# Performance work log

Hardware: AMD Instinct MI355X
Metric: run time of the kernel (lower is better)

The kernel has to match this reference:

```python
import jax, jax.numpy as jnp
import numpy as np

V, D, H, DH, F, L, B, S = 1400, 1024, 16, 64, 4096, 12, 1, 2048
EPS = 1e-5
STD = 0.02


def _layernorm(x, scale, bias):
    m = jnp.mean(x, axis=-1, keepdims=True)
    v = jnp.var(x, axis=-1, keepdims=True)
    return (x - m) * jax.lax.rsqrt(v + EPS) * scale + bias


def _rope_cache(seq_len, d_head):
    inv_freq = 1.0 / (10000.0 ** (jnp.arange(0, d_head, 2, dtype=jnp.float32) / d_head))
    t = jnp.arange(seq_len, dtype=jnp.float32)
    freqs = jnp.outer(t, inv_freq)              # [S, DH/2]
    emb = jnp.concatenate([freqs, freqs], -1)   # [S, DH]
    return jnp.cos(emb), jnp.sin(emb)


def _rotate_half(x):
    x1, x2 = x[..., : x.shape[-1] // 2], x[..., x.shape[-1] // 2 :]
    return jnp.concatenate([-x2, x1], axis=-1)


def _block(x, p, cos, sin, mask):
    Wq, Wk, Wv, Wo, l1s, l1b, l2s, l2b, w1, w2, w3 = p
    b, s, _ = x.shape
    h = _layernorm(x, l1s, l1b)
    q = jnp.einsum('bsd,de->bse', h, Wq).reshape(b, s, H, DH).transpose(0, 2, 1, 3)
    k = jnp.einsum('bsd,de->bse', h, Wk).reshape(b, s, H, DH).transpose(0, 2, 1, 3)
    v = jnp.einsum('bsd,de->bse', h, Wv).reshape(b, s, H, DH).transpose(0, 2, 1, 3)
    c = cos[None, None]  # [1,1,S,DH]
    sn = sin[None, None]
    q = q * c + _rotate_half(q) * sn
    k = k * c + _rotate_half(k) * sn
    scores = jnp.einsum('bhqd,bhkd->bhqk', q, k) / np.sqrt(DH).astype(np.float32)
    scores = jnp.where(mask, scores, -1e9)
    attn = jax.nn.softmax(scores, axis=-1)      # dropout=identity (eval)
    out = jnp.einsum('bhqk,bhkd->bhqd', attn, v)
    out = out.transpose(0, 2, 1, 3).reshape(b, s, D)
    x = x + jnp.einsum('bsd,de->bse', out, Wo)
    h2 = _layernorm(x, l2s, l2b)
    ffn = jnp.einsum('bsf,fd->bsd', jax.nn.silu(jnp.einsum('bsd,df->bsf', h2, w1)) * jnp.einsum('bsd,df->bsf', h2, w3), w2)
    return x + ffn


def _forward(input_ids, tok_emb, Wq, Wk, Wv, Wo, ln1_s, ln1_b, ln2_s, ln2_b, w1, w2, w3, lnf_s, lnf_b, lm_head):
    b, s = input_ids.shape
    x = tok_emb[input_ids]                      # [B,S,D]
    cos, sin = _rope_cache(s, DH)
    mask = jnp.tril(jnp.ones((s, s), dtype=bool))
    blk = jax.checkpoint(lambda c, p: _block(c, p, cos, sin, mask))
    x, _ = jax.lax.scan(lambda c, p: (blk(c, p), None), x,
                        (Wq, Wk, Wv, Wo, ln1_s, ln1_b, ln2_s, ln2_b, w1, w2, w3))
    x = _layernorm(x, lnf_s, lnf_b)
    return jnp.einsum('bsd,dv->bsv', x, lm_head)


def setup_inputs() -> dict:
    key = jax.random.key(0)
    ks = jax.random.split(key, 10)
    inp = {
        'input_ids': jax.random.randint(ks[0], (B, S), 0, V),
        'tok_emb': jax.random.normal(ks[1], (V, D), jnp.float32) * STD,
        'Wq': jax.random.normal(ks[2], (L, D, D), jnp.float32) * STD,
        'Wk': jax.random.normal(ks[3], (L, D, D), jnp.float32) * STD,
        'Wv': jax.random.normal(ks[4], (L, D, D), jnp.float32) * STD,
        'Wo': jax.random.normal(ks[5], (L, D, D), jnp.float32) * STD,
        'ln1_s': jnp.ones((L, D), jnp.float32),
        'ln1_b': jnp.zeros((L, D), jnp.float32),
        'ln2_s': jnp.ones((L, D), jnp.float32),
        'ln2_b': jnp.zeros((L, D), jnp.float32),
        'w1': jax.random.normal(ks[6], (L, D, F), jnp.float32) * STD,
        'w2': jax.random.normal(ks[7], (L, F, D), jnp.float32) * STD,
        'w3': jax.random.normal(ks[8], (L, D, F), jnp.float32) * STD,
        'lnf_s': jnp.ones((D,), jnp.float32),
        'lnf_b': jnp.zeros((D,), jnp.float32),
        'lm_head': jax.random.normal(ks[9], (D, V), jnp.float32) * STD,
    }
    return inp


def reference(input_ids, tok_emb, Wq, Wk, Wv, Wo, ln1_s, ln1_b, ln2_s, ln2_b, w1, w2, w3, lnf_s, lnf_b, lm_head):
    return _forward(input_ids, tok_emb, Wq, Wk, Wv, Wo, ln1_s, ln1_b, ln2_s, ln2_b, w1, w2, w3, lnf_s, lnf_b, lm_head)
```

## Files before the change

### kernel.cpp

```cpp
#include <hip/hip_runtime.h>
#include <math.h>

constexpr int SEQ = 2048;
constexpr int DIM = 1024;
constexpr int NH  = 16;
constexpr int HD  = 64;
constexpr int FF  = 4096;
constexpr int NL  = 12;
constexpr int VOC = 1400;
constexpr int VOCP = 1408;

typedef __bf16 bf16_t;
typedef __bf16 bf16x8 __attribute__((ext_vector_type(8)));
typedef float  f32x4  __attribute__((ext_vector_type(4)));

typedef __attribute__((address_space(1))) const void GV;
typedef __attribute__((address_space(3))) void LV;

__device__ __forceinline__ void gll16(const bf16_t* g, bf16_t* l) {
  __builtin_amdgcn_global_load_lds((GV*)g, (LV*)l, 16, 0, 0);
}

__global__ __launch_bounds__(256) void k_embed(const int* __restrict__ ids,
                                               const float* __restrict__ emb,
                                               float* __restrict__ x) {
  int s = blockIdx.x;
  int d = threadIdx.x * 4;
  const float4 v = *(const float4*)&emb[(size_t)ids[s] * DIM + d];
  *(float4*)&x[(size_t)s * DIM + d] = v;
}

__global__ __launch_bounds__(256) void k_rtab(float* __restrict__ ct,
                                              float* __restrict__ st) {
  int id = blockIdx.x * 256 + threadIdx.x;
  int i = id & 31;
  int s = id >> 5;
  float ang = (float)s * powf(10000.f, -(float)i * (1.f / 32.f));
  float sn, cs;
  sincosf(ang, &sn, &cs);
  ct[id] = cs;
  st[id] = sn;
}

__global__ __launch_bounds__(256) void k_ln(const float* __restrict__ x,
                                            const float* __restrict__ sc,
                                            const float* __restrict__ bi,
                                            bf16_t* __restrict__ out) {
  int s = blockIdx.x * 4 + (threadIdx.x >> 6);
  int l = threadIdx.x & 63;
  const float* xr = x + (size_t)s * DIM;
  float4 v[4];
  float sum = 0.f, sq = 0.f;
#pragma unroll
  for (int i = 0; i < 4; ++i) {
    v[i] = *(const float4*)&xr[i * 256 + l * 4];
#pragma unroll
    for (int j = 0; j < 4; ++j) { sum += v[i][j]; sq += v[i][j] * v[i][j]; }
  }
#pragma unroll
  for (int d = 1; d < 64; d <<= 1) {
    sum += __shfl_xor(sum, d);
    sq  += __shfl_xor(sq, d);
  }
  float mean = sum * (1.f / DIM);
  float var  = sq * (1.f / DIM) - mean * mean;
  float inv  = rsqrtf(var + 1e-5f);
#pragma unroll
  for (int i = 0; i < 4; ++i) {
    int off = i * 256 + l * 4;
    float4 scv = *(const float4*)&sc[off];
    float4 biv = *(const float4*)&bi[off];
#pragma unroll
    for (int j = 0; j < 4; ++j) {
      float o = (v[i][j] - mean) * inv * scv[j] + biv[j];
      out[(size_t)s * DIM + off + j] = (bf16_t)o;
    }
  }
}

__global__ __launch_bounds__(256) void k_cvt_t(const float* __restrict__ src,
                                               bf16_t* __restrict__ dst,
                                               int K_, int N_, int Npad_,
                                               size_t dstride, int imode) {
  __shared__ bf16_t T[64][66];
  const int k0 = blockIdx.y * 64;
  const int n0 = blockIdx.x * 64;
  const size_t so = (size_t)blockIdx.z * K_ * N_;
  const size_t dof = (size_t)blockIdx.z * dstride;
  const int t = threadIdx.x;
  const int kk = t >> 4;
  const int nn = (t & 15) * 4;
#pragma unroll
  for (int it = 0; it < 4; ++it) {
    int krow = kk + it * 16;
    float4 v = {0.f, 0.f, 0.f, 0.f};
    if (n0 + nn < N_) v = *(const float4*)&src[so + (size_t)(k0 + krow) * N_ + n0 + nn];
#pragma unroll
    for (int q = 0; q < 4; ++q) T[nn + q][krow] = (bf16_t)v[q];
  }
  __syncthreads();
#pragma unroll
  for (int it = 0; it < 4; ++it) {
    int c = it * 256 + t;
    int nr = c >> 4;
    int kc = (c & 15) * 4;
    int f = n0 + nr;
    int drow = (imode == 0) ? f : ((f >> 4) * 32 + ((imode == 2) ? 16 : 0) + (f & 15));
    ushort4 o = *(const ushort4*)&T[nr][kc];
    *(ushort4*)&dst[dof + (size_t)drow * K_ + k0 + kc] = o;
  }
}

template <int TM, int TN, int OUTMODE>
__global__ __launch_bounds__(256) void k_gemm2(const bf16_t* __restrict__ A,
                                               const bf16_t* __restrict__ Bt,
                                               float* __restrict__ Cf,
                                               bf16_t* __restrict__ Cb,
                                               bf16_t* __restrict__ aux1,
                                               bf16_t* __restrict__ aux2,
                                               const float* __restrict__ ct,
                                               const float* __restrict__ st,
                                               int M, int N, int K) {
  constexpr int MI = TM / 32;
  constexpr int JN = TN / 32;
  __shared__ bf16_t As[TM * 64];
  __shared__ bf16_t Bs[TN * 64];
  const int t = threadIdx.x;
  const int w = t >> 6, l = t & 63;
  const int h = l >> 4, r16 = l & 15;
  const int m0 = blockIdx.y * TM, n0 = blockIdx.x * TN;
  const int wr = (w >> 1) * (TM / 2);
  const int wc = (w & 1) * (TN / 2);
  const int sr8  = l >> 3;
  const int xch  = ((l & 7) ^ sr8) * 8;
  const int s7   = r16 & 7;

  f32x4 acc[MI][JN] = {};

  const bf16_t* pa = &A[(size_t)(m0 + w * 8 + sr8) * K + xch];
  const bf16_t* pb = &Bt[(size_t)(n0 + w * 8 + sr8) * K + xch];

  for (int k0 = 0; k0 < K; k0 += 64) {
#pragma unroll
    for (int i = 0; i < MI; ++i)
      gll16(pa + (size_t)i * 32 * K + k0, &As[(i * 32 + w * 8) * 64]);
#pragma unroll
    for (int i = 0; i < JN; ++i)
      gll16(pb + (size_t)i * 32 * K + k0, &Bs[(i * 32 + w * 8) * 64]);
    __syncthreads();
#pragma unroll
    for (int kk = 0; kk < 2; ++kk) {
      const int p = ((kk * 4 + h) ^ s7) * 8;
      bf16x8 af[MI], bfr[JN];
#pragma unroll
      for (int i = 0; i < MI; ++i)
        af[i] = *(const bf16x8*)&As[(wr + i * 16 + r16) * 64 + p];
#pragma unroll
      for (int j = 0; j < JN; ++j)
        bfr[j] = *(const bf16x8*)&Bs[(wc + j * 16 + r16) * 64 + p];
#pragma unroll
      for (int i = 0; i < MI; ++i)
#pragma unroll
        for (int j = 0; j < JN; ++j)
          acc[i][j] = __builtin_amdgcn_mfma_f32_16x16x32_bf16(af[i], bfr[j], acc[i][j], 0, 0, 0);
    }
    __syncthreads();
  }

  if constexpr (OUTMODE == 4) {
    const int reg = n0 >> 10;
    const int cbase = (n0 & 1023) + wc;
    if (reg == 2) {
#pragma unroll
      for (int i = 0; i < MI; ++i)
#pragma unroll
        for (int j = 0; j < JN; ++j)
#pragma unroll
          for (int r = 0; r < 4; ++r) {
            int row = m0 + wr + i * 16 + h * 4 + r;
            Cb[(size_t)row * DIM + cbase + j * 16 + r16] = (bf16_t)acc[i][j][r];
          }
    } else {
      bf16_t* dst = reg ? aux2 : aux1;
#pragma unroll
      for (int i = 0; i < MI; ++i)
#pragma unroll
        for (int r = 0; r < 4; ++r) {
          int row = m0 + wr + i * 16 + h * 4 + r;
          float c0 = ct[row * 32 + r16],      s0 = st[row * 32 + r16];
          float c1 = ct[row * 32 + 16 + r16], s1 = st[row * 32 + 16 + r16];
          float lo0 = acc[i][0][r], hi0 = acc[i][2][r];
          float lo1 = acc[i][1][r], hi1 = acc[i][3][r];
          size_t rb = (size_t)row * DIM + cbase;
          dst[rb + r16]      = (bf16_t)(lo0 * c0 - hi0 * s0);
          dst[rb + 32 + r16] = (bf16_t)(hi0 * c0 + lo0 * s0);
          dst[rb + 16 + r16] = (bf16_t)(lo1 * c1 - hi1 * s1);
          dst[rb + 48 + r16] = (bf16_t)(hi1 * c1 + lo1 * s1);
        }
    }
  } else if constexpr (OUTMODE == 6) {
    const int fbase = ((n0 + wc) >> 5) * 16;
#pragma unroll
    for (int i = 0; i < MI; ++i)
#pragma unroll
      for (int r = 0; r < 4; ++r) {
        int row = m0 + wr + i * 16 + h * 4 + r;
        float a0 = acc[i][0][r], b0 = acc[i][1][r];
        float a1 = acc[i][2][r], b1 = acc[i][3][r];
        float g0 = a0 / (1.f + expf(-a0)) * b0;
        float g1v = a1 / (1.f + expf(-a1)) * b1;
        size_t rb = (size_t)row * FF + fbase;
        aux1[rb + r16]      = (bf16_t)g0;
        aux1[rb + 16 + r16] = (bf16_t)g1v;
      }
  } else {
#pragma unroll
    for (int i = 0; i < MI; ++i)
#pragma unroll
      for (int j = 0; j < JN; ++j)
#pragma unroll
        for (int r = 0; r < 4; ++r) {
          int row = m0 + wr + i * 16 + h * 4 + r;
          int col = n0 + wc + j * 16 + r16;
          if (col < N) {
            float vv = acc[i][j][r];
            size_t idx = (size_t)row * N + col;
            if (OUTMODE == 0) Cf[idx] = vv;
            else Cf[idx] += vv;
          }
        }
  }
}

__global__ __launch_bounds__(512, 1) void k_gemm256_gate(const bf16_t* __restrict__ A,
                                                         const bf16_t* __restrict__ Bt,
                                                         bf16_t* __restrict__ gate,
                                                         int K) {
  __shared__ bf16_t As[2][256 * 64];
  __shared__ bf16_t Bs[2][256 * 64];
  const int t = threadIdx.x;
  const int w = t >> 6, l = t & 63;
  const int h = l >> 4, r16 = l & 15;
  const int m0 = blockIdx.y * 256, n0 = blockIdx.x * 256;
  const int wr = (w >> 2) * 128;
  const int wc = (w & 3) * 64;
  const int sr = t >> 3;
  const int xch = ((t & 7) ^ (sr & 7)) * 8;
  const int s7 = r16 & 7;

  f32x4 acc[8][4] = {};

  const bf16_t* pa = &A[(size_t)(m0 + sr) * K + xch];
  const bf16_t* pb = &Bt[(size_t)(n0 + sr) * K + xch];
  const int NT = K >> 6;

  auto STAGE = [&](int kt, int b) {
    const int k0 = kt << 6;
    bf16_t* baseA = &As[b][(w * 8) * 64];
    bf16_t* baseB = &Bs[b][(w * 8) * 64];
#pragma unroll
    for (int i = 0; i < 4; ++i) {
      gll16(pa + (size_t)(i * 64) * K + k0, baseA + i * 64 * 64);
      gll16(pb + (size_t)(i * 64) * K + k0, baseB + i * 64 * 64);
    }
  };

  STAGE(0, 0);
  asm volatile("s_waitcnt vmcnt(0)" ::: "memory");
  __builtin_amdgcn_s_barrier();
  __builtin_amdgcn_sched_barrier(0);

  int cur = 0;
  for (int tt = 0; tt < NT; ++tt) {
    if (tt + 1 < NT) STAGE(tt + 1, cur ^ 1);
#pragma unroll
    for (int kk = 0; kk < 2; ++kk) {
      const int p = ((kk * 4 + h) ^ s7) * 8;
      bf16x8 af[8], bfr[4];
#pragma unroll
      for (int i = 0; i < 8; ++i)
        af[i] = *(const bf16x8*)&As[cur][(wr + i * 16 + r16) * 64 + p];
#pragma unroll
      for (int j = 0; j < 4; ++j)
        bfr[j] = *(const bf16x8*)&Bs[cur][(wc + j * 16 + r16) * 64 + p];
#pragma unroll
      for (int i = 0; i < 8; ++i)
#pragma unroll
        for (int j = 0; j < 4; ++j)
          acc[i][j] = __builtin_amdgcn_mfma_f32_16x16x32_bf16(af[i], bfr[j], acc[i][j], 0, 0, 0);
    }
    asm volatile("s_waitcnt vmcnt(0)" ::: "memory");
    __builtin_amdgcn_s_barrier();
    __builtin_amdgcn_sched_barrier(0);
    cur ^= 1;
  }

  const int fbase = ((n0 + wc) >> 5) * 16;
#pragma unroll
  for (int i = 0; i < 8; ++i)
#pragma unroll
    for (int r = 0; r < 4; ++r) {
      int row = m0 + wr + i * 16 + h * 4 + r;
      float a0 = acc[i][0][r], b0 = acc[i][1][r];
      float a1 = acc[i][2][r], b1 = acc[i][3][r];
      float g0 = a0 / (1.f + expf(-a0)) * b0;
      float g1v = a1 / (1.f + expf(-a1)) * b1;
      size_t rb = (size_t)row * FF + fbase;
      gate[rb + r16]      = (bf16_t)g0;
      gate[rb + 16 + r16] = (bf16_t)g1v;
    }
}

__global__ __launch_bounds__(256) void k_attn4(const bf16_t* __restrict__ qb,
                                               const bf16_t* __restrict__ kb,
                                               const bf16_t* __restrict__ vb,
                                               bf16_t* __restrict__ ao) {
  __shared__ bf16_t Ks[64][72];
  __shared__ bf16_t Vt[64][72];
  __shared__ bf16_t Pl[4][16][72];
  const int raw = blockIdx.x;
  const int head = blockIdx.y;
  const int qt = (head < 8) ? raw : (31 - raw);
  const int t = threadIdx.x;
  const int w = t >> 6, l = t & 63;
  const int h = l >> 4, r16 = l & 15;
  const size_t hoff = (size_t)head * HD;
  const int srow = t >> 2;
  const int ssg  = (t & 3) * 8;

  const int q0 = qt * 64 + w * 16;
  const int q_abs = q0 + r16;

  bf16x8 aq[2];
#pragma unroll
  for (int c = 0; c < 2; ++c)
    aq[c] = *(const bf16x8*)&qb[(size_t)(q0 + r16) * DIM + hoff + c * 32 + h * 8];

  f32x4 o[4] = {};
  float mrun = -1e30f, lrun = 0.f;

  const int kend = qt * 64 + 63;
  for (int k0 = 0; k0 <= kend; k0 += 64) {
#pragma unroll
    for (int it = 0; it < 2; ++it) {
      bf16x8 kv = *(const bf16x8*)&kb[(size_t)(k0 + srow) * DIM + hoff + ssg + it * 32];
      *(bf16x8*)&Ks[srow][ssg + it * 32] = kv;
    }
#pragma unroll
    for (int it = 0; it < 2; ++it) {
      bf16x8 vv = *(const bf16x8*)&vb[(size_t)(k0 + srow) * DIM + hoff + ssg + it * 32];
#pragma unroll
      for (int j = 0; j < 8; ++j) Vt[ssg + it * 32 + j][srow] = vv[j];
    }
    __syncthreads();

    if (k0 <= q0 + 15) {
      f32x4 sc[4];
      __builtin_amdgcn_s_setprio(1);
#pragma unroll
      for (int tc = 0; tc < 4; ++tc) {
        f32x4 z = {};
        bf16x8 a0 = *(const bf16x8*)&Ks[tc * 16 + r16][h * 8];
        bf16x8 a1 = *(const bf16x8*)&Ks[tc * 16 + r16][32 + h * 8];
        z = __builtin_amdgcn_mfma_f32_16x16x32_bf16(a0, aq[0], z, 0, 0, 0);
        z = __builtin_amdgcn_mfma_f32_16x16x32_bf16(a1, aq[1], z, 0, 0, 0);
        sc[tc] = z;
      }
      __builtin_amdgcn_s_setprio(0);
      float pmax = -1e30f;
#pragma unroll
      for (int tc = 0; tc < 4; ++tc)
#pragma unroll
        for (int r = 0; r < 4; ++r) {
          int key = k0 + tc * 16 + h * 4 + r;
          float v = sc[tc][r] * 0.125f;
          if (key > q_abs) v = -1e30f;
          sc[tc][r] = v;
          pmax = fmaxf(pmax, v);
        }
      pmax = fmaxf(pmax, __shfl_xor(pmax, 16));
      pmax = fmaxf(pmax, __shfl_xor(pmax, 32));
      float mnew = fmaxf(mrun, pmax);
      float alpha = expf(mrun - mnew);
      mrun = mnew;
      float ssum = 0.f;
#pragma unroll
      for (int tc = 0; tc < 4; ++tc)
#pragma unroll
        for (int r = 0; r < 4; ++r) {
          float pv = expf(sc[tc][r] - mnew);
          sc[tc][r] = pv;
          ssum += pv;
        }
      ssum += __shfl_xor(ssum, 16);
      ssum += __shfl_xor(ssum, 32);
      lrun = lrun * alpha + ssum;
#pragma unroll
      for (int tc = 0; tc < 4; ++tc)
#pragma unroll
        for (int r = 0; r < 4; ++r)
          Pl[w][r16][tc * 16 + h * 4 + r] = (bf16_t)sc[tc][r];
      float ar[4];
#pragma unroll
      for (int r = 0; r < 4; ++r) ar[r] = __shfl(alpha, h * 4 + r);
#pragma unroll
      for (int cti = 0; cti < 4; ++cti)
#pragma unroll
        for (int r = 0; r < 4; ++r) o[cti][r] *= ar[r];
      bf16x8 pa0 = *(const bf16x8*)&Pl[w][r16][h * 8];
      bf16x8 pa1 = *(const bf16x8*)&Pl[w][r16][32 + h * 8];
      __builtin_amdgcn_s_setprio(1);
#pragma unroll
      for (int cti = 0; cti < 4; ++cti) {
        bf16x8 v0 = *(const bf16x8*)&Vt[cti * 16 + r16][h * 8];
        bf16x8 v1 = *(const bf16x8*)&Vt[cti * 16 + r16][32 + h * 8];
        o[cti] = __builtin_amdgcn_mfma_f32_16x16x32_bf16(pa0, v0, o[cti], 0, 0, 0);
        o[cti] = __builtin_amdgcn_mfma_f32_16x16x32_bf16(pa1, v1, o[cti], 0, 0, 0);
      }
      __builtin_amdgcn_s_setprio(0);
    }
    __syncthreads();
  }
  float lr[4];
#pragma unroll
  for (int r = 0; r < 4; ++r) lr[r] = __shfl(lrun, h * 4 + r);
#pragma unroll
  for (int cti = 0; cti < 4; ++cti)
#pragma unroll
    for (int r = 0; r < 4; ++r) {
      int row = q0 + h * 4 + r;
      ao[(size_t)row * DIM + hoff + cti * 16 + r16] = (bf16_t)(o[cti][r] / lr[r]);
    }
}

extern "C" void kernel_launch(void* const* d_in, const int* in_sizes, int n_in,
                              void* d_out, int out_size, void* d_ws, size_t ws_size,
                              hipStream_t stream) {
  const int*   ids  = (const int*)d_in[0];
  const float* temb = (const float*)d_in[1];
  const float* Wq   = (const float*)d_in[2];
  const float* Wk   = (const float*)d_in[3];
  const float* Wv   = (const float*)d_in[4];
  const float* Wo   = (const float*)d_in[5];
  const float* ln1s = (const float*)d_in[6];
  const float* ln1b = (const float*)d_in[7];
  const float* ln2s = (const float*)d_in[8];
  const float* ln2b = (const float*)d_in[9];
  const float* w1   = (const float*)d_in[10];
  const float* w2   = (const float*)d_in[11];
  const float* w3   = (const float*)d_in[12];
  const float* lnfs = (const float*)d_in[13];
  const float* lnfb = (const float*)d_in[14];
  const float* lmh  = (const float*)d_in[15];
  float* out = (float*)d_out;

  char* p = (char*)d_ws;
  size_t used = 0;
  auto alloc = [&](size_t bytes) {
    void* r = (void*)p;
    size_t a = (bytes + 255) & ~(size_t)255;
    p += a; used += a;
    return r;
  };
  float*  x     = (float*)alloc((size_t)SEQ * DIM * 4);
  bf16_t* hb    = (bf16_t*)alloc((size_t)SEQ * DIM * 2);
  bf16_t* qb2   = (bf16_t*)alloc((size_t)SEQ * DIM * 2);
  bf16_t* kb2   = (bf16_t*)alloc((size_t)SEQ * DIM * 2);
  bf16_t* vb2   = (bf16_t*)alloc((size_t)SEQ * DIM * 2);
  bf16_t* aob   = (bf16_t*)alloc((size_t)SEQ * DIM * 2);
  bf16_t* gateb = (bf16_t*)alloc((size_t)SEQ * FF * 2);
  float*  ctab  = (float*)alloc((size_t)SEQ * 32 * 4);
  float*  stab  = (float*)alloc((size_t)SEQ * 32 * 4);

  const size_t szDD = (size_t)DIM * DIM;
  const size_t szDF = (size_t)DIM * FF;
  const size_t wt_bytes = ((size_t)NL * (3 * szDD + szDD + 2 * szDF + szDF) + (size_t)VOCP * DIM) * 2;
  const bool bigws = (ws_size >= used + wt_bytes + (1u << 20));

  bf16_t *bQKV, *bWo, *bW13, *bw2, *blm, *wscratch = nullptr;
  if (bigws) {
    bQKV = (bf16_t*)alloc(NL * 3 * szDD * 2);
    bWo  = (bf16_t*)alloc(NL * szDD * 2);
    bW13 = (bf16_t*)alloc(NL * 2 * szDF * 2);
    bw2  = (bf16_t*)alloc(NL * szDF * 2);
    blm  = (bf16_t*)alloc((size_t)VOCP * DIM * 2);
  } else {
    wscratch = (bf16_t*)alloc(2 * szDF * 2);
    bQKV = bWo = bW13 = bw2 = blm = wscratch;
  }

  auto cvt = [&](const float* src, bf16_t* dst, int K_, int N_, int Npad_, int nz,
                 size_t dstride, int imode) {
    dim3 g(Npad_ / 64, K_ / 64, nz);
    k_cvt_t<<<g, 256, 0, stream>>>(src, dst, K_, N_, Npad_, dstride, imode);
  };

  if (bigws) {
    cvt(Wq, bQKV,             DIM, DIM, DIM, NL, 3 * szDD, 0);
    cvt(Wk, bQKV + szDD,      DIM, DIM, DIM, NL, 3 * szDD, 0);
    cvt(Wv, bQKV + 2 * szDD,  DIM, DIM, DIM, NL, 3 * szDD, 0);
    cvt(Wo, bWo,              DIM, DIM, DIM, NL, szDD, 0);
    cvt(w1, bW13,             DIM, FF,  FF,  NL, 2 * szDF, 1);
    cvt(w3, bW13,             DIM, FF,  FF,  NL, 2 * szDF, 2);
    cvt(w2, bw2,              FF,  DIM, DIM, NL, szDF, 0);
    cvt(lmh, blm,             DIM, VOC, VOCP, 1, 0, 0);
  }
  auto wpQKV = [&](int lyr) -> bf16_t* {
    if (bigws) return bQKV + (size_t)lyr * 3 * szDD;
    cvt(Wq + (size_t)lyr * szDD, wscratch,            DIM, DIM, DIM, 1, 0, 0);
    cvt(Wk + (size_t)lyr * szDD, wscratch + szDD,     DIM, DIM, DIM, 1, 0, 0);
    cvt(Wv + (size_t)lyr * szDD, wscratch + 2 * szDD, DIM, DIM, DIM, 1, 0, 0);
    return wscratch;
  };
  auto wpW13 = [&](int lyr) -> bf16_t* {
    if (bigws) return bW13 + (size_t)lyr * 2 * szDF;
    cvt(w1 + (size_t)lyr * szDF, wscratch, DIM, FF, FF, 1, 0, 1);
    cvt(w3 + (size_t)lyr * szDF, wscratch, DIM, FF, FF, 1, 0, 2);
    return wscratch;
  };
  auto wp1 = [&](bf16_t* big, const float* src, int lyr, int K_, int N_, int Npad_) -> bf16_t* {
    if (bigws) return big + (size_t)lyr * Npad_ * K_;
    cvt(src + (size_t)lyr * K_ * N_, wscratch, K_, N_, Npad_, 1, 0, 0);
    return wscratch;
  };

  k_rtab<<<(SEQ * 32) / 256, 256, 0, stream>>>(ctab, stab);
  k_embed<<<SEQ, 256, 0, stream>>>(ids, temb, x);

  dim3 gQKV(3 * DIM / 128, SEQ / 64);
  dim3 gDD(DIM / 64, SEQ / 64);
  dim3 gW13(2 * FF / 256, SEQ / 256);
  dim3 gLM(VOCP / 64, SEQ / 64);
  dim3 gAt(32, NH);

  for (int l = 0; l < NL; ++l) {
    k_ln<<<SEQ / 4, 256, 0, stream>>>(x, ln1s + (size_t)l * DIM, ln1b + (size_t)l * DIM, hb);
    k_gemm2<64, 128, 4><<<gQKV, 256, 0, stream>>>(hb, wpQKV(l), nullptr, vb2, qb2, kb2,
                                                  ctab, stab, SEQ, 3 * DIM, DIM);
    k_attn4<<<gAt, 256, 0, stream>>>(qb2, kb2, vb2, aob);
    k_gemm2<64, 64, 2><<<gDD, 256, 0, stream>>>(aob, wp1(bWo, Wo, l, DIM, DIM, DIM), x, nullptr,
                                                nullptr, nullptr, nullptr, nullptr, SEQ, DIM, DIM);
    k_ln<<<SEQ / 4, 256, 0, stream>>>(x, ln2s + (size_t)l * DIM, ln2b + (size_t)l * DIM, hb);
    k_gemm256_gate<<<gW13, 512, 0, stream>>>(hb, wpW13(l), gateb, DIM);
    k_gemm2<64, 64, 2><<<gDD, 256, 0, stream>>>(gateb, wp1(bw2, w2, l, FF, DIM, DIM), x, nullptr,
                                                nullptr, nullptr, nullptr, nullptr, SEQ, DIM, FF);
  }
  k_ln<<<SEQ / 4, 256, 0, stream>>>(x, lnfs, lnfb, hb);
  k_gemm2<64, 64, 0><<<gLM, 256, 0, stream>>>(hb, bigws ? blm : wp1(blm, lmh, 0, DIM, VOC, VOCP),
                                              out, nullptr, nullptr, nullptr, nullptr, nullptr,
                                              SEQ, VOC, DIM);
}
```

Baseline: 2.892 ms.

## Use 128-key tiles and register-prefetch next K/V tile in attention kernel

The causal flash-attention kernel now processes 128 keys per iteration instead of 64, halving the number of block-wide barriers and online-softmax rescale steps. The next K/V tile is loaded into registers right after the barrier, so global loads overlap with the current tile's MFMA and softmax work. This costs more LDS and registers per block, which may lower occupancy. It also wastes more masked work on the diagonal tile, and tiles with odd 64-row counts mask a full extra half-tile.

```diff
diff --git a/kernel.cpp b/kernel.cpp
--- a/kernel.cpp
+++ b/kernel.cpp
@@ -315,9 +315,9 @@
                                                const bf16_t* __restrict__ kb,
                                                const bf16_t* __restrict__ vb,
                                                bf16_t* __restrict__ ao) {
-  __shared__ bf16_t Ks[64][72];
-  __shared__ bf16_t Vt[64][72];
-  __shared__ bf16_t Pl[4][16][72];
+  __shared__ bf16_t Ks[128][72];
+  __shared__ bf16_t Vt[64][136];
+  __shared__ bf16_t Pl[4][16][136];
   const int raw = blockIdx.x;
   const int head = blockIdx.y;
   const int qt = (head < 8) ? raw : (31 - raw);
@@ -325,8 +325,8 @@
   const int w = t >> 6, l = t & 63;
   const int h = l >> 4, r16 = l & 15;
   const size_t hoff = (size_t)head * HD;
-  const int srow = t >> 2;
-  const int ssg  = (t & 3) * 8;
+  const int srow = t >> 1;
+  const int sc4  = (t & 1) * 4;
 
   const int q0 = qt * 64 + w * 16;
   const int q_abs = q0 + r16;
@@ -340,25 +340,38 @@
   float mrun = -1e30f, lrun = 0.f;
 
   const int kend = qt * 64 + 63;
-  for (int k0 = 0; k0 <= kend; k0 += 64) {
-#pragma unroll
-    for (int it = 0; it < 2; ++it) {
-      bf16x8 kv = *(const bf16x8*)&kb[(size_t)(k0 + srow) * DIM + hoff + ssg + it * 32];
-      *(bf16x8*)&Ks[srow][ssg + it * 32] = kv;
-    }
-#pragma unroll
-    for (int it = 0; it < 2; ++it) {
-      bf16x8 vv = *(const bf16x8*)&vb[(size_t)(k0 + srow) * DIM + hoff + ssg + it * 32];
-#pragma unroll
-      for (int j = 0; j < 8; ++j) Vt[ssg + it * 32 + j][srow] = vv[j];
-    }
+
+  bf16x8 kreg[4], vreg[4];
+#pragma unroll
+  for (int it = 0; it < 4; ++it) {
+    kreg[it] = *(const bf16x8*)&kb[(size_t)srow * DIM + hoff + (sc4 + it) * 8];
+    vreg[it] = *(const bf16x8*)&vb[(size_t)srow * DIM + hoff + (sc4 + it) * 8];
+  }
+
+  for (int k0 = 0; k0 <= kend; k0 += 128) {
+#pragma unroll
+    for (int it = 0; it < 4; ++it)
+      *(bf16x8*)&Ks[srow][(sc4 + it) * 8] = kreg[it];
+#pragma unroll
+    for (int it = 0; it < 4; ++it)
+#pragma unroll
+      for (int j = 0; j < 8; ++j) Vt[(sc4 + it) * 8 + j][srow] = vreg[it][j];
     __syncthreads();
 
+    if (k0 + 128 <= kend) {
+      const size_t nb = (size_t)(k0 + 128 + srow) * DIM + hoff;
+#pragma unroll
+      for (int it = 0; it < 4; ++it) {
+        kreg[it] = *(const bf16x8*)&kb[nb + (sc4 + it) * 8];
+        vreg[it] = *(const bf16x8*)&vb[nb + (sc4 + it) * 8];
+      }
+    }
+
     if (k0 <= q0 + 15) {
-      f32x4 sc[4];
+      f32x4 sc[8];
       __builtin_amdgcn_s_setprio(1);
 #pragma unroll
-      for (int tc = 0; tc < 4; ++tc) {
+      for (int tc = 0; tc < 8; ++tc) {
         f32x4 z = {};
         bf16x8 a0 = *(const bf16x8*)&Ks[tc * 16 + r16][h * 8];
         bf16x8 a1 = *(const bf16x8*)&Ks[tc * 16 + r16][32 + h * 8];
@@ -369,7 +382,7 @@
       __builtin_amdgcn_s_setprio(0);
       float pmax = -1e30f;
 #pragma unroll
-      for (int tc = 0; tc < 4; ++tc)
+      for (int tc = 0; tc < 8; ++tc)
 #pragma unroll
         for (int r = 0; r < 4; ++r) {
           int key = k0 + tc * 16 + h * 4 + r;
@@ -385,7 +398,7 @@
       mrun = mnew;
       float ssum = 0.f;
 #pragma unroll
-      for (int tc = 0; tc < 4; ++tc)
+      for (int tc = 0; tc < 8; ++tc)
 #pragma unroll
         for (int r = 0; r < 4; ++r) {
           float pv = expf(sc[tc][r] - mnew);
@@ -396,7 +409,7 @@
       ssum += __shfl_xor(ssum, 32);
       lrun = lrun * alpha + ssum;
 #pragma unroll
-      for (int tc = 0; tc < 4; ++tc)
+      for (int tc = 0; tc < 8; ++tc)
 #pragma unroll
         for (int r = 0; r < 4; ++r)
           Pl[w][r16][tc * 16 + h * 4 + r] = (bf16_t)sc[tc][r];
@@ -407,15 +420,15 @@
       for (int cti = 0; cti < 4; ++cti)
 #pragma unroll
         for (int r = 0; r < 4; ++r) o[cti][r] *= ar[r];
-      bf16x8 pa0 = *(const bf16x8*)&Pl[w][r16][h * 8];
-      bf16x8 pa1 = *(const bf16x8*)&Pl[w][r16][32 + h * 8];
       __builtin_amdgcn_s_setprio(1);
 #pragma unroll
-      for (int cti = 0; cti < 4; ++cti) {
-        bf16x8 v0 = *(const bf16x8*)&Vt[cti * 16 + r16][h * 8];
-        bf16x8 v1 = *(const bf16x8*)&Vt[cti * 16 + r16][32 + h * 8];
-        o[cti] = __builtin_amdgcn_mfma_f32_16x16x32_bf16(pa0, v0, o[cti], 0, 0, 0);
-        o[cti] = __builtin_amdgcn_mfma_f32_16x16x32_bf16(pa1, v1, o[cti], 0, 0, 0);
+      for (int ks = 0; ks < 4; ++ks) {
+        bf16x8 pk = *(const bf16x8*)&Pl[w][r16][ks * 32 + h * 8];
+#pragma unroll
+        for (int cti = 0; cti < 4; ++cti) {
+          bf16x8 vv = *(const bf16x8*)&Vt[cti * 16 + r16][ks * 32 + h * 8];
+          o[cti] = __builtin_amdgcn_mfma_f32_16x16x32_bf16(pk, vv, o[cti], 0, 0, 0);
+        }
       }
       __builtin_amdgcn_s_setprio(0);
     }
```

Result: faster. 2.724 ms (-5.8%).
